# Optimization experiments

Measured on AMD Instinct MI355X. Metric: run time of the kernel, lower is better.

## Reference

```python
import jax, jax.numpy as jnp
import numpy as np

NUM_ROI = 400
N_GRAPHS = 128
N_NODES = NUM_ROI * N_GRAPHS            # 51200
N_EDGES = N_NODES * 40                  # 2048000
EMB = [128, 128]
BN_EPS = 1e-5


def mish(x):
    return x * jnp.tanh(jax.nn.softplus(x))


def gcn_conv(x, row, col, ew, W, b, n_nodes):
    """PyG GCNConv: h = XW; add self-loops (w=1); sym-normalize; scatter-add; + bias."""
    h = x @ W                                            # [N, out]
    loops = jnp.arange(n_nodes, dtype=row.dtype)
    row_ = jnp.concatenate([row, loops])
    col_ = jnp.concatenate([col, loops])
    ew_ = jnp.concatenate([ew, jnp.ones((n_nodes,), ew.dtype)])
    deg = jax.ops.segment_sum(ew_, col_, num_segments=n_nodes)
    dinv = jnp.where(deg > 0, jax.lax.rsqrt(deg), 0.0)
    norm = dinv[row_] * ew_ * dinv[col_]                 # [E+N]
    msg = norm[:, None] * h[row_]                        # gather + scale
    out = jax.ops.segment_sum(msg, col_, num_segments=n_nodes)
    return out + b


def setup_inputs() -> dict:
    key = jax.random.key(0)
    ks = jax.random.split(key, 16)
    inp = {
        "x": jax.random.normal(ks[0], (N_NODES, NUM_ROI), jnp.float32),
        "edge_index": jax.random.randint(ks[1], (2, N_EDGES), 0, N_NODES, jnp.int64)
        if jax.config.jax_enable_x64 else jax.random.randint(ks[1], (2, N_EDGES), 0, N_NODES, jnp.int32),
        "edge_attr": jax.random.uniform(ks[2], (N_EDGES,), jnp.float32),
        "batch": jnp.repeat(jnp.arange(N_GRAPHS), NUM_ROI),
        "conv1_w": jax.random.normal(ks[3], (NUM_ROI, EMB[0]), jnp.float32) * 0.05,
        "conv1_b": jax.random.normal(ks[4], (EMB[0],), jnp.float32) * 0.05,
        "conv2_w": jax.random.normal(ks[5], (EMB[0], EMB[1]), jnp.float32) * 0.05,
        "conv2_b": jax.random.normal(ks[6], (EMB[1],), jnp.float32) * 0.05,
        "ro_w": jax.random.normal(ks[7], (EMB[1], 8), jnp.float32) * 0.05,
        "ro_b": jax.random.normal(ks[8], (8,), jnp.float32) * 0.05,
        "fc1_w": jax.random.normal(ks[9], (8 * NUM_ROI, NUM_ROI), jnp.float32) * 0.02,
        "fc1_b": jax.random.normal(ks[10], (NUM_ROI,), jnp.float32) * 0.02,
        "bn_gamma": jnp.ones((NUM_ROI,), jnp.float32),
        "bn_beta": jnp.zeros((NUM_ROI,), jnp.float32),
        "fc2_w": jax.random.normal(ks[11], (NUM_ROI, 2), jnp.float32) * 0.05,
        "fc2_b": jax.random.normal(ks[12], (2,), jnp.float32) * 0.05,
    }
    return inp


def reference(x, edge_index, edge_attr, batch,
              conv1_w, conv1_b, conv2_w, conv2_b,
              ro_w, ro_b, fc1_w, fc1_b, bn_gamma, bn_beta, fc2_w, fc2_b):
    n = x.shape[0]
    row, col = edge_index[0], edge_index[1]
    h = mish(gcn_conv(x, row, col, edge_attr, conv1_w, conv1_b, n))
    h = mish(gcn_conv(h, row, col, edge_attr, conv2_w, conv2_b, n))
    out = mish(h @ ro_w + ro_b)                          # [N, 8]
    feats = out.reshape(-1, NUM_ROI * 8)                 # [B, 3200]
    z = feats @ fc1_w + fc1_b                            # [B, 400]
    # BatchNorm1d (training mode: batch statistics, biased variance)
    mu = jnp.mean(z, axis=0)
    var = jnp.mean((z - mu) ** 2, axis=0)
    zn = (z - mu) * jax.lax.rsqrt(var + BN_EPS) * bn_gamma + bn_beta
    logits = mish(zn) @ fc2_w + fc2_b                    # [B, 2]
    return logits
```

## Files before the change

kernel.cpp:

```cpp
#include <hip/hip_runtime.h>
#include <hip/hip_fp16.h>
#include <math.h>

#define NN 51200
#define NE 2048000
#define F 128
#define NB 1000
#define EPB 2048
#define NBKT 200
#define ECAP 12288

typedef _Float16 half8 __attribute__((ext_vector_type(8)));
typedef float floatx4 __attribute__((ext_vector_type(4)));

__device__ __forceinline__ float mish_f(float x) {
  if (x > 20.0f) return x;
  float e = __expf(x);
  float w = 1.0f + e;
  w = w * w;
  return x * (w - 1.0f) / (w + 1.0f);
}

__global__ __launch_bounds__(256) void k_icsort(const int* __restrict__ ei, const float* __restrict__ ew,
                                                unsigned* __restrict__ gcnt, uint2* __restrict__ E,
                                                const float* __restrict__ W1, const float* __restrict__ W2,
                                                _Float16* __restrict__ Wt1, _Float16* __restrict__ Wt2,
                                                float* __restrict__ z) {
  int bid = blockIdx.x, t = threadIdx.x;
  if (bid < NB) {
    __shared__ uint2 ebuf[EPB];
    __shared__ unsigned char bkt[EPB];
    __shared__ unsigned hist[NBKT];
    __shared__ unsigned base[NBKT];
    for (int i = t; i < NBKT; i += 256) hist[i] = 0u;
    __syncthreads();
    int off0 = bid * EPB;
    for (int it = 0; it < EPB; it += 256) {
      int e = off0 + it + t;
      int dst = ei[NE + e];
      int src = ei[e];
      float w = ew[e];
      ebuf[it + t] = make_uint2((unsigned)src | ((unsigned)(dst & 255) << 16), __float_as_uint(w));
      int b = dst >> 8;
      bkt[it + t] = (unsigned char)b;
      atomicAdd(&hist[b], 1u);
    }
    __syncthreads();
    for (int i = t; i < NBKT; i += 256)
      base[i] = (unsigned)i * ECAP + atomicAdd(&gcnt[i], hist[i]);
    __syncthreads();
    for (int it = 0; it < EPB; it += 256) {
      int j = it + t;
      unsigned b = bkt[j];
      unsigned pos = atomicAdd(&base[b], 1u);
      E[pos] = ebuf[j];
    }
  } else {
    int idx = (bid - NB) * 256 + t;
    if (idx < 51200) {
      int k = idx >> 7, n = idx & 127;
      Wt1[n * 400 + k] = (_Float16)W1[idx];
      z[idx] = 0.0f;
    } else {
      int i2 = idx - 51200;
      int k = i2 >> 7, n = i2 & 127;
      Wt2[n * 128 + k] = (_Float16)W2[i2];
    }
  }
}

__global__ __launch_bounds__(1024) void k_fprep(const uint2* __restrict__ E, const unsigned* __restrict__ btot,
                                                int2* __restrict__ bounds, float* __restrict__ dinv,
                                                unsigned* __restrict__ csr) {
  __shared__ unsigned lc[256];
  __shared__ float ld[256];
  __shared__ int curs[256];
  __shared__ int ws4[4];
  int b = blockIdx.x, t = threadIdx.x;
  if (t < 256) {
    lc[t] = 0u;
    ld[t] = 0.f;
  }
  __syncthreads();
  unsigned e0 = (unsigned)b * ECAP, e1 = e0 + btot[b];
  for (unsigned e = e0 + t; e < e1; e += 1024) {
    uint2 v = E[e];
    unsigned node = (v.x >> 16) & 255u;
    atomicAdd(&lc[node], 1u);
    atomicAdd(&ld[node], __uint_as_float(v.y));
  }
  __syncthreads();
  int lane = t & 63, wid = (t >> 6) & 3;
  int cv = (t < 256) ? (int)lc[t] : 0;
  int x = cv;
#pragma unroll
  for (int off = 1; off < 64; off <<= 1) {
    int y = __shfl_up(x, off);
    if (lane >= off) x += y;
  }
  if (t < 256 && lane == 63) ws4[wid] = x;
  __syncthreads();
  if (t < 256) {
    int woff = 0;
    for (int k = 0; k < wid; ++k) woff += ws4[k];
    int start = (int)e0 + woff + x - cv;
    bounds[b * 256 + t] = make_int2(start, start + cv);
    dinv[b * 256 + t] = rsqrtf(ld[t] + 1.0f);
    curs[t] = start;
  }
  __syncthreads();
  for (unsigned e = e0 + t; e < e1; e += 1024) {
    uint2 v = E[e];
    unsigned node = (v.x >> 16) & 255u;
    unsigned src = v.x & 0xFFFFu;
    int p = atomicAdd(&curs[node], 1);
    unsigned pk = src | ((unsigned)__half_as_ushort(__float2half_rn(__uint_as_float(v.y))) << 16);
    csr[p] = pk;
  }
}

template <bool A_IS_F32>
__global__ __launch_bounds__(256) void k_gemm16(const void* __restrict__ Av,
                                                const _Float16* __restrict__ Wt,
                                                const float* __restrict__ dinv,
                                                __half* __restrict__ C, int K) {
  __shared__ _Float16 As[128][40];
  __shared__ _Float16 Bs[128][40];
  int t = threadIdx.x;
  int bm = blockIdx.x * 128;
  int w = t >> 6, l = t & 63, rr = l & 15, q = l >> 4;
  int si = t >> 1, sj = (t & 1) * 16;

  floatx4 acc[2][8];
#pragma unroll
  for (int a = 0; a < 2; ++a)
#pragma unroll
    for (int b = 0; b < 8; ++b) acc[a][b] = (floatx4){0.f, 0.f, 0.f, 0.f};

  for (int k0 = 0; k0 < K; k0 += 32) {
    if (A_IS_F32) {
      const float* A = (const float*)Av;
      half8 h0, h1;
      if (k0 + sj < K) {
        const float* ap = A + (size_t)(bm + si) * K + k0 + sj;
        float4 v0 = *(const float4*)(ap + 0);
        float4 v1 = *(const float4*)(ap + 4);
        float4 v2 = *(const float4*)(ap + 8);
        float4 v3 = *(const float4*)(ap + 12);
        h0 = (half8){(_Float16)v0.x, (_Float16)v0.y, (_Float16)v0.z, (_Float16)v0.w,
                     (_Float16)v1.x, (_Float16)v1.y, (_Float16)v1.z, (_Float16)v1.w};
        h1 = (half8){(_Float16)v2.x, (_Float16)v2.y, (_Float16)v2.z, (_Float16)v2.w,
                     (_Float16)v3.x, (_Float16)v3.y, (_Float16)v3.z, (_Float16)v3.w};
      } else {
        h0 = (half8){0, 0, 0, 0, 0, 0, 0, 0};
        h1 = h0;
      }
      *(half8*)&As[si][sj] = h0;
      *(half8*)&As[si][sj + 8] = h1;
    } else {
      const __half* A = (const __half*)Av;
      uint4 u0, u1;
      if (k0 + sj < K) {
        const __half* ap = A + (size_t)(bm + si) * K + k0 + sj;
        u0 = *(const uint4*)ap;
        u1 = *(const uint4*)(ap + 8);
      } else {
        u0 = make_uint4(0, 0, 0, 0);
        u1 = u0;
      }
      *(uint4*)&As[si][sj] = u0;
      *(uint4*)&As[si][sj + 8] = u1;
    }
    {
      uint4 u0, u1;
      if (k0 + sj < K) {
        const _Float16* wp = Wt + (size_t)si * K + k0 + sj;
        u0 = *(const uint4*)wp;
        u1 = *(const uint4*)(wp + 8);
      } else {
        u0 = make_uint4(0, 0, 0, 0);
        u1 = u0;
      }
      *(uint4*)&Bs[si][sj] = u0;
      *(uint4*)&Bs[si][sj + 8] = u1;
    }
    __syncthreads();

    half8 a0 = *(const half8*)&As[w * 32 + rr][q * 8];
    half8 a1 = *(const half8*)&As[w * 32 + 16 + rr][q * 8];
#pragma unroll
    for (int nt = 0; nt < 8; ++nt) {
      half8 b = *(const half8*)&Bs[nt * 16 + rr][q * 8];
      acc[0][nt] = __builtin_amdgcn_mfma_f32_16x16x32_f16(a0, b, acc[0][nt], 0, 0, 0);
      acc[1][nt] = __builtin_amdgcn_mfma_f32_16x16x32_f16(a1, b, acc[1][nt], 0, 0, 0);
    }
    __syncthreads();
  }
#pragma unroll
  for (int mt = 0; mt < 2; ++mt) {
    float dv[4];
#pragma unroll
    for (int r4 = 0; r4 < 4; ++r4) dv[r4] = dinv[bm + w * 32 + mt * 16 + q * 4 + r4];
#pragma unroll
    for (int nt = 0; nt < 8; ++nt)
#pragma unroll
      for (int r4 = 0; r4 < 4; ++r4) {
        int row = bm + w * 32 + mt * 16 + q * 4 + r4;
        C[(size_t)row * 128 + nt * 16 + rr] = __float2half(dv[r4] * acc[mt][nt][r4]);
      }
  }
}

__global__ __launch_bounds__(256) void k_agg(const __half2* __restrict__ h, const int2* __restrict__ bounds,
                                             const unsigned* __restrict__ csr, const float* __restrict__ dinv,
                                             const float* __restrict__ bias, __half2* __restrict__ out) {
  unsigned lane = threadIdx.x & 63u;
  int n = blockIdx.x * 4 + (threadIdx.x >> 6);
  float di = dinv[n];
  float2 self = __half22float2(h[((unsigned)n << 6) + lane]);
  float sx = 0.f, sy = 0.f;
  int2 bd = bounds[n];
  int p = __builtin_amdgcn_readfirstlane(bd.x);
  int p1 = __builtin_amdgcn_readfirstlane(bd.y);
  for (; p + 16 <= p1; p += 16) {
    unsigned c[16];
#pragma unroll
    for (int u = 0; u < 16; ++u) c[u] = csr[p + u];
    float2 f[16];
#pragma unroll
    for (int u = 0; u < 16; ++u) f[u] = __half22float2(h[((c[u] & 0xFFFFu) << 6) + lane]);
#pragma unroll
    for (int u = 0; u < 16; ++u) {
      float w = __half2float(__ushort_as_half((unsigned short)(c[u] >> 16)));
      sx += w * f[u].x;
      sy += w * f[u].y;
    }
  }
  for (; p + 4 <= p1; p += 4) {
    unsigned c[4];
#pragma unroll
    for (int u = 0; u < 4; ++u) c[u] = csr[p + u];
    float2 f[4];
#pragma unroll
    for (int u = 0; u < 4; ++u) f[u] = __half22float2(h[((c[u] & 0xFFFFu) << 6) + lane]);
#pragma unroll
    for (int u = 0; u < 4; ++u) {
      float w = __half2float(__ushort_as_half((unsigned short)(c[u] >> 16)));
      sx += w * f[u].x;
      sy += w * f[u].y;
    }
  }
  for (; p < p1; ++p) {
    unsigned c0 = csr[p];
    float2 f0 = __half22float2(h[((c0 & 0xFFFFu) << 6) + lane]);
    float w = __half2float(__ushort_as_half((unsigned short)(c0 >> 16)));
    sx += w * f0.x;
    sy += w * f0.y;
  }
  float2 bb = ((const float2*)bias)[lane];
  float ax = di * (sx + self.x) + bb.x;
  float ay = di * (sy + self.y) + bb.y;
  out[((unsigned)n << 6) + lane] = __floats2half2_rn(mish_f(ax), mish_f(ay));
}

__global__ __launch_bounds__(256) void k_agg2ro(const __half2* __restrict__ h, const int2* __restrict__ bounds,
                                                const unsigned* __restrict__ csr, const float* __restrict__ dinv,
                                                const float* __restrict__ bias, const float* __restrict__ rw,
                                                const float* __restrict__ rb, float* __restrict__ o8) {
  __shared__ float2 wl2[8][64];
  int t = threadIdx.x;
  for (int i = t; i < 512; i += 256) {
    int k = i >> 6, l = i & 63;
    wl2[k][l] = make_float2(rw[(2 * l) * 8 + k], rw[(2 * l + 1) * 8 + k]);
  }
  __syncthreads();
  unsigned lane = t & 63u;
  int n = blockIdx.x * 4 + (t >> 6);
  float di = dinv[n];
  float2 self = __half22float2(h[((unsigned)n << 6) + lane]);
  float sx = 0.f, sy = 0.f;
  int2 bd = bounds[n];
  int p = __builtin_amdgcn_readfirstlane(bd.x);
  int p1 = __builtin_amdgcn_readfirstlane(bd.y);
  for (; p + 16 <= p1; p += 16) {
    unsigned c[16];
#pragma unroll
    for (int u = 0; u < 16; ++u) c[u] = csr[p + u];
    float2 f[16];
#pragma unroll
    for (int u = 0; u < 16; ++u) f[u] = __half22float2(h[((c[u] & 0xFFFFu) << 6) + lane]);
#pragma unroll
    for (int u = 0; u < 16; ++u) {
      float w = __half2float(__ushort_as_half((unsigned short)(c[u] >> 16)));
      sx += w * f[u].x;
      sy += w * f[u].y;
    }
  }
  for (; p + 4 <= p1; p += 4) {
    unsigned c[4];
#pragma unroll
    for (int u = 0; u < 4; ++u) c[u] = csr[p + u];
    float2 f[4];
#pragma unroll
    for (int u = 0; u < 4; ++u) f[u] = __half22float2(h[((c[u] & 0xFFFFu) << 6) + lane]);
#pragma unroll
    for (int u = 0; u < 4; ++u) {
      float w = __half2float(__ushort_as_half((unsigned short)(c[u] >> 16)));
      sx += w * f[u].x;
      sy += w * f[u].y;
    }
  }
  for (; p < p1; ++p) {
    unsigned c0 = csr[p];
    float2 f0 = __half22float2(h[((c0 & 0xFFFFu) << 6) + lane]);
    float w = __half2float(__ushort_as_half((unsigned short)(c0 >> 16)));
    sx += w * f0.x;
    sy += w * f0.y;
  }
  float2 bb = ((const float2*)bias)[lane];
  float m0 = mish_f(di * (sx + self.x) + bb.x);
  float m1 = mish_f(di * (sy + self.y) + bb.y);
  float p8[8];
#pragma unroll
  for (int k = 0; k < 8; ++k) {
    float2 wv = wl2[k][lane];
    p8[k] = m0 * wv.x + m1 * wv.y;
  }
  bool b5 = (lane & 32u) != 0u, b4 = (lane & 16u) != 0u, b3 = (lane & 8u) != 0u;
  float q4[4];
#pragma unroll
  for (int j = 0; j < 4; ++j) {
    float send = b5 ? p8[j] : p8[j + 4];
    float r = __shfl_xor(send, 32);
    q4[j] = (b5 ? p8[j + 4] : p8[j]) + r;
  }
  float q2[2];
#pragma unroll
  for (int j = 0; j < 2; ++j) {
    float send = b4 ? q4[j] : q4[j + 2];
    float r = __shfl_xor(send, 16);
    q2[j] = (b4 ? q4[j + 2] : q4[j]) + r;
  }
  float v;
  {
    float send = b3 ? q2[0] : q2[1];
    float r = __shfl_xor(send, 8);
    v = (b3 ? q2[1] : q2[0]) + r;
  }
  v += __shfl_xor(v, 1);
  v += __shfl_xor(v, 2);
  v += __shfl_xor(v, 4);
  if ((lane & 7u) == 0u) {
    int k = (int)(lane >> 3);
    o8[(size_t)n * 8 + k] = mish_f(v + rb[k]);
  }
}

__global__ __launch_bounds__(448) void k_fc1(const float* __restrict__ feats, const float* __restrict__ w,
                                             float* __restrict__ z) {
  __shared__ float fs[8][128];
  int t = threadIdx.x;
  int kc = blockIdx.x * 128;
  int g0 = blockIdx.y * 8;
  for (int i = t; i < 1024; i += 448) {
    int g = i >> 7, k = i & 127;
    fs[g][k] = feats[(size_t)(g0 + g) * 3200 + kc + k];
  }
  __syncthreads();
  if (t < 400) {
    float a[8];
#pragma unroll
    for (int g = 0; g < 8; ++g) a[g] = 0.0f;
    for (int k = 0; k < 128; ++k) {
      float wv = w[(size_t)(kc + k) * 400 + t];
#pragma unroll
      for (int g = 0; g < 8; ++g) a[g] += fs[g][k] * wv;
    }
#pragma unroll
    for (int g = 0; g < 8; ++g) atomicAdd(&z[(size_t)(g0 + g) * 400 + t], a[g]);
  }
}

__global__ __launch_bounds__(128) void k_bn(const float* __restrict__ z, const float* __restrict__ gamma,
                                            const float* __restrict__ beta, float* __restrict__ gs,
                                            float* __restrict__ gb) {
  int j = blockIdx.x;
  int b = threadIdx.x;
  float v = z[b * 400 + j];
  float s = v, s2 = v * v;
#pragma unroll
  for (int off = 1; off < 64; off <<= 1) {
    s += __shfl_xor(s, off);
    s2 += __shfl_xor(s2, off);
  }
  __shared__ float ls[2], ls2[2];
  if ((b & 63) == 0) {
    ls[b >> 6] = s;
    ls2[b >> 6] = s2;
  }
  __syncthreads();
  if (b == 0) {
    float mu = (ls[0] + ls[1]) * (1.0f / 128.0f);
    float var = (ls2[0] + ls2[1]) * (1.0f / 128.0f) - mu * mu;
    float rs = rsqrtf(var + 1e-5f);
    float g = gamma[j] * rs;
    gs[j] = g;
    gb[j] = beta[j] - mu * g;
  }
}

__global__ __launch_bounds__(256) void k_fc2(const float* __restrict__ z, const float* __restrict__ gs,
                                             const float* __restrict__ gb, const float* __restrict__ w2,
                                             const float* __restrict__ b2, float* __restrict__ out) {
  int bg = blockIdx.x;
  int t = threadIdx.x;
  float a0 = 0.f, a1 = 0.f;
  for (int j = t; j < 400; j += 256) {
    float zn = z[bg * 400 + j] * gs[j] + gb[j];
    float m = mish_f(zn);
    a0 += m * w2[j * 2];
    a1 += m * w2[j * 2 + 1];
  }
#pragma unroll
  for (int off = 1; off < 64; off <<= 1) {
    a0 += __shfl_xor(a0, off);
    a1 += __shfl_xor(a1, off);
  }
  __shared__ float s0[4], s1[4];
  if ((t & 63) == 0) {
    s0[t >> 6] = a0;
    s1[t >> 6] = a1;
  }
  __syncthreads();
  if (t == 0) {
    out[bg * 2 + 0] = b2[0] + s0[0] + s0[1] + s0[2] + s0[3];
    out[bg * 2 + 1] = b2[1] + s1[0] + s1[1] + s1[2] + s1[3];
  }
}

extern "C" void kernel_launch(void* const* d_in, const int* in_sizes, int n_in,
                              void* d_out, int out_size, void* d_ws, size_t ws_size,
                              hipStream_t stream) {
  (void)in_sizes; (void)n_in; (void)out_size; (void)ws_size;
  const float* x   = (const float*)d_in[0];
  const int*   ei  = (const int*)d_in[1];
  const float* ew  = (const float*)d_in[2];
  const float* c1w = (const float*)d_in[4];
  const float* c1b = (const float*)d_in[5];
  const float* c2w = (const float*)d_in[6];
  const float* c2b = (const float*)d_in[7];
  const float* rw  = (const float*)d_in[8];
  const float* rb  = (const float*)d_in[9];
  const float* f1w = (const float*)d_in[10];
  const float* bng = (const float*)d_in[12];
  const float* bnb = (const float*)d_in[13];
  const float* f2w = (const float*)d_in[14];
  const float* f2b = (const float*)d_in[15];
  float* out = (float*)d_out;

  char* ws = (char*)d_ws;
  size_t off = 0;
  auto alloc = [&](size_t bytes) {
    void* p = ws + off;
    off = (off + bytes + 255) & ~(size_t)255;
    return p;
  };
  float* dinv    = (float*)alloc((size_t)NN * 4);
  int2*  bounds  = (int2*)alloc((size_t)NN * 8);
  unsigned* gcnt = (unsigned*)alloc(NBKT * 4);
  unsigned* csr  = (unsigned*)alloc((size_t)NBKT * ECAP * 4);
  __half* A1     = (__half*)alloc((size_t)NN * F * 2);
  __half* B1     = (__half*)alloc((size_t)NN * F * 2);
  _Float16* Wt1  = (_Float16*)alloc((size_t)400 * 128 * 2);
  _Float16* Wt2  = (_Float16*)alloc((size_t)128 * 128 * 2);
  float* o8      = (float*)alloc((size_t)NN * 8 * 4);
  float* z       = (float*)alloc((size_t)128 * 400 * 4);
  float* gs      = (float*)alloc(400 * 4);
  float* gb      = (float*)alloc(400 * 4);

  uint2* E = (uint2*)A1;

  hipMemsetAsync(gcnt, 0, NBKT * 4, stream);
  k_icsort<<<NB + 264, 256, 0, stream>>>(ei, ew, gcnt, E, c1w, c2w, Wt1, Wt2, z);
  k_fprep<<<NBKT, 1024, 0, stream>>>(E, gcnt, bounds, dinv, csr);

  k_gemm16<true><<<NN / 128, 256, 0, stream>>>(x, Wt1, dinv, A1, 400);
  k_agg<<<NN / 4, 256, 0, stream>>>((const __half2*)A1, bounds, csr, dinv, c1b, (__half2*)B1);
  k_gemm16<false><<<NN / 128, 256, 0, stream>>>(B1, Wt2, dinv, A1, 128);
  k_agg2ro<<<NN / 4, 256, 0, stream>>>((const __half2*)A1, bounds, csr, dinv, c2b, rw, rb, o8);

  {
    dim3 g(25, 16);
    k_fc1<<<g, 448, 0, stream>>>(o8, f1w, z);
  }
  k_bn<<<400, 128, 0, stream>>>(z, bng, bnb, gs, gb);
  k_fc2<<<128, 256, 0, stream>>>(z, gs, gb, f2w, f2b, out);
}
```

Before: 401.7 us.

## Move fc1 to fp16 MFMA with split-K partials instead of atomics

Replaces the scalar FP32 fc1 kernel, which accumulated with atomics, by an MFMA 16x16x32 fp16 GEMM. The fc1 weight is transposed to fp16 inside the existing preprocessing kernel and the readout features are stored in fp16. Split-K writes four partial buffers, which BN and fc2 now sum, so the z zeroing and the atomics go away. This trades fp16 precision loss in the fc1 inputs for matrix-core throughput, and adds an extra 2.5MB weight transpose on every call.

```diff
diff --git a/kernel.cpp b/kernel.cpp
--- a/kernel.cpp
+++ b/kernel.cpp
@@ -9,6 +9,7 @@
 #define EPB 2048
 #define NBKT 200
 #define ECAP 12288
+#define TRB 250
 
 typedef _Float16 half8 __attribute__((ext_vector_type(8)));
 typedef float floatx4 __attribute__((ext_vector_type(4)));
@@ -25,7 +26,7 @@
                                                 unsigned* __restrict__ gcnt, uint2* __restrict__ E,
                                                 const float* __restrict__ W1, const float* __restrict__ W2,
                                                 _Float16* __restrict__ Wt1, _Float16* __restrict__ Wt2,
-                                                float* __restrict__ z) {
+                                                const float* __restrict__ f1w, _Float16* __restrict__ Wtf) {
   int bid = blockIdx.x, t = threadIdx.x;
   if (bid < NB) {
     __shared__ uint2 ebuf[EPB];
@@ -55,16 +56,25 @@
       unsigned pos = atomicAdd(&base[b], 1u);
       E[pos] = ebuf[j];
     }
-  } else {
+  } else if (bid < NB + 264) {
     int idx = (bid - NB) * 256 + t;
     if (idx < 51200) {
       int k = idx >> 7, n = idx & 127;
       Wt1[n * 400 + k] = (_Float16)W1[idx];
-      z[idx] = 0.0f;
     } else {
       int i2 = idx - 51200;
       int k = i2 >> 7, n = i2 & 127;
       Wt2[n * 128 + k] = (_Float16)W2[i2];
+    }
+  } else {
+    int tb = bid - (NB + 264);
+    int n0 = (tb % 25) * 16;
+    int k0 = (tb / 25) * 320;
+    int n = t & 15, kk = t >> 4;
+#pragma unroll 4
+    for (int i = 0; i < 20; ++i) {
+      int k = k0 + kk * 20 + i;
+      Wtf[(size_t)(n0 + n) * 3200 + k] = (_Float16)f1w[(size_t)k * 400 + n0 + n];
     }
   }
 }
@@ -266,7 +276,7 @@
 __global__ __launch_bounds__(256) void k_agg2ro(const __half2* __restrict__ h, const int2* __restrict__ bounds,
                                                 const unsigned* __restrict__ csr, const float* __restrict__ dinv,
                                                 const float* __restrict__ bias, const float* __restrict__ rw,
-                                                const float* __restrict__ rb, float* __restrict__ o8) {
+                                                const float* __restrict__ rb, __half* __restrict__ o8h) {
   __shared__ float2 wl2[8][64];
   int t = threadIdx.x;
   for (int i = t; i < 512; i += 256) {
@@ -352,41 +362,54 @@
   v += __shfl_xor(v, 4);
   if ((lane & 7u) == 0u) {
     int k = (int)(lane >> 3);
-    o8[(size_t)n * 8 + k] = mish_f(v + rb[k]);
-  }
-}
-
-__global__ __launch_bounds__(448) void k_fc1(const float* __restrict__ feats, const float* __restrict__ w,
-                                             float* __restrict__ z) {
-  __shared__ float fs[8][128];
+    o8h[(size_t)n * 8 + k] = __float2half(mish_f(v + rb[k]));
+  }
+}
+
+__global__ __launch_bounds__(256) void k_fc1m(const __half* __restrict__ A, const _Float16* __restrict__ Bt,
+                                              float* __restrict__ zp) {
+  __shared__ _Float16 As[128][40];
+  __shared__ _Float16 Bs[16][40];
   int t = threadIdx.x;
-  int kc = blockIdx.x * 128;
-  int g0 = blockIdx.y * 8;
-  for (int i = t; i < 1024; i += 448) {
-    int g = i >> 7, k = i & 127;
-    fs[g][k] = feats[(size_t)(g0 + g) * 3200 + kc + k];
-  }
-  __syncthreads();
-  if (t < 400) {
-    float a[8];
-#pragma unroll
-    for (int g = 0; g < 8; ++g) a[g] = 0.0f;
-    for (int k = 0; k < 128; ++k) {
-      float wv = w[(size_t)(kc + k) * 400 + t];
-#pragma unroll
-      for (int g = 0; g < 8; ++g) a[g] += fs[g][k] * wv;
-    }
-#pragma unroll
-    for (int g = 0; g < 8; ++g) atomicAdd(&z[(size_t)(g0 + g) * 400 + t], a[g]);
-  }
-}
-
-__global__ __launch_bounds__(128) void k_bn(const float* __restrict__ z, const float* __restrict__ gamma,
+  int n0 = blockIdx.x * 16;
+  int kbase = blockIdx.y * 800;
+  int w = t >> 6, l = t & 63, rr = l & 15, q = l >> 4;
+  int si = t >> 1, sj = (t & 1) * 16;
+  floatx4 acc[2];
+  acc[0] = (floatx4){0.f, 0.f, 0.f, 0.f};
+  acc[1] = (floatx4){0.f, 0.f, 0.f, 0.f};
+  for (int k0 = kbase; k0 < kbase + 800; k0 += 32) {
+    *(uint4*)&As[si][sj] = *(const uint4*)(A + (size_t)si * 3200 + k0 + sj);
+    *(uint4*)&As[si][sj + 8] = *(const uint4*)(A + (size_t)si * 3200 + k0 + sj + 8);
+    if (t < 64) {
+      int ni = t >> 2, s2 = (t & 3) * 8;
+      *(uint4*)&Bs[ni][s2] = *(const uint4*)(Bt + (size_t)(n0 + ni) * 3200 + k0 + s2);
+    }
+    __syncthreads();
+    half8 a0 = *(const half8*)&As[w * 32 + rr][q * 8];
+    half8 a1 = *(const half8*)&As[w * 32 + 16 + rr][q * 8];
+    half8 b = *(const half8*)&Bs[rr][q * 8];
+    acc[0] = __builtin_amdgcn_mfma_f32_16x16x32_f16(a0, b, acc[0], 0, 0, 0);
+    acc[1] = __builtin_amdgcn_mfma_f32_16x16x32_f16(a1, b, acc[1], 0, 0, 0);
+    __syncthreads();
+  }
+  float* zo = zp + (size_t)blockIdx.y * 51200;
+#pragma unroll
+  for (int mt = 0; mt < 2; ++mt)
+#pragma unroll
+    for (int r4 = 0; r4 < 4; ++r4) {
+      int row = w * 32 + mt * 16 + q * 4 + r4;
+      zo[row * 400 + n0 + rr] = acc[mt][r4];
+    }
+}
+
+__global__ __launch_bounds__(128) void k_bn(const float* __restrict__ zp, const float* __restrict__ gamma,
                                             const float* __restrict__ beta, float* __restrict__ gs,
                                             float* __restrict__ gb) {
   int j = blockIdx.x;
   int b = threadIdx.x;
-  float v = z[b * 400 + j];
+  int idx = b * 400 + j;
+  float v = zp[idx] + zp[51200 + idx] + zp[102400 + idx] + zp[153600 + idx];
   float s = v, s2 = v * v;
 #pragma unroll
   for (int off = 1; off < 64; off <<= 1) {
@@ -409,14 +432,16 @@
   }
 }
 
-__global__ __launch_bounds__(256) void k_fc2(const float* __restrict__ z, const float* __restrict__ gs,
+__global__ __launch_bounds__(256) void k_fc2(const float* __restrict__ zp, const float* __restrict__ gs,
                                              const float* __restrict__ gb, const float* __restrict__ w2,
                                              const float* __restrict__ b2, float* __restrict__ out) {
   int bg = blockIdx.x;
   int t = threadIdx.x;
   float a0 = 0.f, a1 = 0.f;
   for (int j = t; j < 400; j += 256) {
-    float zn = z[bg * 400 + j] * gs[j] + gb[j];
+    int idx = bg * 400 + j;
+    float zv = zp[idx] + zp[51200 + idx] + zp[102400 + idx] + zp[153600 + idx];
+    float zn = zv * gs[j] + gb[j];
     float m = mish_f(zn);
     a0 += m * w2[j * 2];
     a1 += m * w2[j * 2 + 1];
@@ -473,26 +498,27 @@
   __half* B1     = (__half*)alloc((size_t)NN * F * 2);
   _Float16* Wt1  = (_Float16*)alloc((size_t)400 * 128 * 2);
   _Float16* Wt2  = (_Float16*)alloc((size_t)128 * 128 * 2);
-  float* o8      = (float*)alloc((size_t)NN * 8 * 4);
-  float* z       = (float*)alloc((size_t)128 * 400 * 4);
+  _Float16* Wtf  = (_Float16*)alloc((size_t)400 * 3200 * 2);
+  __half* o8h    = (__half*)alloc((size_t)NN * 8 * 2);
+  float* zp      = (float*)alloc((size_t)4 * 128 * 400 * 4);
   float* gs      = (float*)alloc(400 * 4);
   float* gb      = (float*)alloc(400 * 4);
 
   uint2* E = (uint2*)A1;
 
   hipMemsetAsync(gcnt, 0, NBKT * 4, stream);
-  k_icsort<<<NB + 264, 256, 0, stream>>>(ei, ew, gcnt, E, c1w, c2w, Wt1, Wt2, z);
+  k_icsort<<<NB + 264 + TRB, 256, 0, stream>>>(ei, ew, gcnt, E, c1w, c2w, Wt1, Wt2, f1w, Wtf);
   k_fprep<<<NBKT, 1024, 0, stream>>>(E, gcnt, bounds, dinv, csr);
 
   k_gemm16<true><<<NN / 128, 256, 0, stream>>>(x, Wt1, dinv, A1, 400);
   k_agg<<<NN / 4, 256, 0, stream>>>((const __half2*)A1, bounds, csr, dinv, c1b, (__half2*)B1);
   k_gemm16<false><<<NN / 128, 256, 0, stream>>>(B1, Wt2, dinv, A1, 128);
-  k_agg2ro<<<NN / 4, 256, 0, stream>>>((const __half2*)A1, bounds, csr, dinv, c2b, rw, rb, o8);
+  k_agg2ro<<<NN / 4, 256, 0, stream>>>((const __half2*)A1, bounds, csr, dinv, c2b, rw, rb, o8h);
 
   {
-    dim3 g(25, 16);
-    k_fc1<<<g, 448, 0, stream>>>(o8, f1w, z);
-  }
-  k_bn<<<400, 128, 0, stream>>>(z, bng, bnb, gs, gb);
-  k_fc2<<<128, 256, 0, stream>>>(z, gs, gb, f2w, f2b, out);
-}
+    dim3 g(25, 4);
+    k_fc1m<<<g, 256, 0, stream>>>(o8h, Wtf, zp);
+  }
+  k_bn<<<400, 128, 0, stream>>>(zp, bng, bnb, gs, gb);
+  k_fc2<<<128, 256, 0, stream>>>(zp, gs, gb, f2w, f2b, out);
+}
```

Measured after the change: 399.4 us. Within noise of the previous version (-0.6%).
